# Optimization experiments

Measured on AMD Instinct MI355X. Metric: run time of the kernel, lower is better.

Reference implementation:

```python
import jax, jax.numpy as jnp
import numpy as np

T = 8          # number of adapter tasks
H = 1024       # hidden_size
I = 4096       # intermediate_size (bert dense input)
D = H // 16    # adapter bottleneck (reduction_factor=16)
B, S = 8, 512
EPS = 1e-12    # BERT LayerNorm eps


def _layernorm(x, g, b):
    mu = jnp.mean(x, axis=-1, keepdims=True)
    var = jnp.mean(jnp.square(x - mu), axis=-1, keepdims=True)
    return (x - mu) * jax.lax.rsqrt(var + EPS) * g + b


def setup_inputs() -> dict:
    key = jax.random.key(0)
    ks = jax.random.split(key, 14)
    std = 0.02
    inp = {
        "hidden_states": jax.random.normal(ks[0], (B, S, I), jnp.float32),
        "input_tensor": jax.random.normal(ks[1], (B, S, H), jnp.float32),
        "dense_w": jax.random.normal(ks[2], (H, I), jnp.float32) * std,
        "dense_b": jnp.zeros((H,), jnp.float32),
        "ln_g": jnp.ones((H,), jnp.float32),
        "ln_b": jnp.zeros((H,), jnp.float32),
        "down_w": jax.random.normal(ks[3], (T, D, H), jnp.float32) * std,
        "down_b": jnp.zeros((T, D), jnp.float32),
        "up_w": jax.random.normal(ks[4], (T, H, D), jnp.float32) * std,
        "up_b": jnp.zeros((T, H), jnp.float32),
        "key_w": jax.random.normal(ks[5], (H, H), jnp.float32) * std,
        "key_b": jnp.zeros((H,), jnp.float32),
        "query_w": jax.random.normal(ks[6], (H, H), jnp.float32) * std,
        "query_b": jnp.zeros((H,), jnp.float32),
        # value init: near-zero with identity diagonal
        "value_w": jnp.full((H, H), 1e-6, jnp.float32).at[jnp.arange(H), jnp.arange(H)].set(1.0),
    }
    return inp


def reference(hidden_states, input_tensor, dense_w, dense_b, ln_g, ln_b,
              down_w, down_b, up_w, up_b, key_w, key_b, query_w, query_b, value_w):
    # dense: [B,S,I] @ [H,I]^T -> [B,S,H]   (dropout = identity in eval)
    h = jnp.einsum('bsi,hi->bsh', hidden_states, dense_w) + dense_b
    prenorm = input_tensor + h
    adapter_in = _layernorm(prenorm, ln_g, ln_b)
    # batched per-task adapters: down-project, relu, up-project -> [T,B,S,H]
    down = jax.nn.relu(jnp.einsum('bsh,tdh->tbsd', adapter_in, down_w)
                       + down_b[:, None, None, :])
    adapter_out = jnp.einsum('tbsd,thd->tbsh', down, up_w) + up_b[:, None, None, :]
    # fusion attention over task axis T
    key = jnp.einsum('tbsh,kh->tbsk', adapter_out, key_w) + key_b
    value = jnp.einsum('tbsh,vh->tbsv', adapter_out + h[None], value_w)
    query = jnp.einsum('bsh,qh->bsq', prenorm, query_w) + query_b
    scores = jnp.sum(query[None] * key, axis=-1, keepdims=True)  # [T,B,S,1]
    probs = jax.nn.softmax(scores, axis=0)
    fusion = jnp.sum(probs * value, axis=0)                       # [B,S,H]
    return _layernorm(input_tensor + fusion, ln_g, ln_b)
```

## Files before the change

### kernel.cpp

```cpp
#include <hip/hip_runtime.h>
#include <cstdint>
#include <cstddef>

typedef float   f32x4 __attribute__((ext_vector_type(4)));
typedef _Float16 f16x8 __attribute__((ext_vector_type(8)));
typedef _Float16 f16x4 __attribute__((ext_vector_type(4)));

#define TOK  4096
#define HID  1024
#define IDIM 4096

#define GLDS16(gp, lp) __builtin_amdgcn_global_load_lds(                      \
    (const __attribute__((address_space(1))) void*)(gp),                      \
    (__attribute__((address_space(3))) void*)(lp), 16, 0, 0)


__global__ __launch_bounds__(256, 4) void gemm_dense(
    const _Float16* __restrict__ A, const _Float16* __restrict__ B,
    int K, int Kchunk, float* __restrict__ part, size_t zstride)
{
    __shared__ _Float16 lA[2][4096];
    __shared__ _Float16 lB[2][4096];
    const int tid  = threadIdx.x;
    const int lane = tid & 63;
    const int wave = tid >> 6;
    const int m0   = blockIdx.x * 128;
    const int n0   = blockIdx.y * 128;
    const int kz0  = blockIdx.z * Kchunk;
    const int wM   = (wave & 1) * 64;
    const int wN   = (wave >> 1) * 64;

    const int srow = lane >> 2;
    const int scol = ((lane & 3) ^ ((lane >> 3) & 3)) * 8;
    const _Float16* gA0 = A + (size_t)(m0 + wave * 32 + srow) * K + kz0 + scol;
    const _Float16* gA1 = gA0 + (size_t)16 * K;
    const _Float16* gB0 = B + (size_t)(n0 + wave * 32 + srow) * K + kz0 + scol;
    const _Float16* gB1 = gB0 + (size_t)16 * K;
    const int soff = wave * 1024;

    f32x4 acc[4][4] = {};
    const int fr  = lane & 15;
    const int khr = lane >> 4;
    const int kxo = (khr ^ ((fr >> 1) & 3)) * 8;

    GLDS16(gA0, &lA[0][soff]);
    GLDS16(gA1, &lA[0][soff + 512]);
    GLDS16(gB0, &lB[0][soff]);
    GLDS16(gB1, &lB[0][soff + 512]);
    __syncthreads();

    int cur = 0;
    for (int k = 0; k < Kchunk; k += 32) {
        if (k + 32 < Kchunk) {
            const int nb = cur ^ 1;
            GLDS16(gA0 + k + 32, &lA[nb][soff]);
            GLDS16(gA1 + k + 32, &lA[nb][soff + 512]);
            GLDS16(gB0 + k + 32, &lB[nb][soff]);
            GLDS16(gB1 + k + 32, &lB[nb][soff + 512]);
        }
        f16x8 afr[4], bfr[4];
#pragma unroll
        for (int mi = 0; mi < 4; ++mi)
            afr[mi] = *(const f16x8*)(&lA[cur][(wM + mi * 16 + fr) * 32 + kxo]);
#pragma unroll
        for (int ni = 0; ni < 4; ++ni)
            bfr[ni] = *(const f16x8*)(&lB[cur][(wN + ni * 16 + fr) * 32 + kxo]);
#pragma unroll
        for (int mi = 0; mi < 4; ++mi)
#pragma unroll
            for (int ni = 0; ni < 4; ++ni)
                acc[mi][ni] = __builtin_amdgcn_mfma_f32_16x16x32_f16(
                    afr[mi], bfr[ni], acc[mi][ni], 0, 0, 0);
        __syncthreads();
        cur ^= 1;
    }

    float* dst = part + (size_t)blockIdx.z * zstride;
    const int cn = lane & 15;
    const int rq = (lane >> 4) * 4;
#pragma unroll
    for (int mi = 0; mi < 4; ++mi)
#pragma unroll
        for (int r = 0; r < 4; ++r) {
            const int m = m0 + wM + mi * 16 + rq + r;
#pragma unroll
            for (int ni = 0; ni < 4; ++ni) {
                const int n = n0 + wN + ni * 16 + cn;
                dst[(size_t)m * HID + n] = acc[mi][ni][r];
            }
        }
}

__global__ __launch_bounds__(256) void reduce_sk(
    const float* __restrict__ in, size_t zstride4, int sk,
    _Float16* __restrict__ outp, int n4)
{
    const int gid = blockIdx.x * 256 + threadIdx.x;
    const int gsz = gridDim.x * 256;
    for (int i = gid; i < n4; i += gsz) {
        f32x4 v = ((const f32x4*)in)[i];
        for (int z = 1; z < sk; ++z)
            v += ((const f32x4*)in)[z * zstride4 + i];
        f16x4 o;
        o[0] = (_Float16)v[0]; o[1] = (_Float16)v[1];
        o[2] = (_Float16)v[2]; o[3] = (_Float16)v[3];
        ((f16x4*)outp)[i] = o;
    }
}

template <int MODE>
__global__ __launch_bounds__(1024, 4) void gemm_w32(
    const _Float16* __restrict__ Ah, const _Float16* __restrict__ B,
    int K, int Ncols,
    float* __restrict__ outF, _Float16* __restrict__ outH,
    const float* __restrict__ bias, const float* __restrict__ addv,
    const float* __restrict__ probs, const float* __restrict__ upb,
    const _Float16* __restrict__ A2, const _Float16* __restrict__ B2,
    _Float16* __restrict__ outH2)
{
    __shared__ _Float16 lA[2][8192];
    __shared__ _Float16 lB[2][8192];
    const int tid  = threadIdx.x;
    const int lane = tid & 63;
    const int wave = tid >> 6;
    const int m0   = blockIdx.x * 128;
    int n0, half = 0;
    const _Float16* Ap = Ah;
    const _Float16* Bp = B;
    if constexpr (MODE == 5) {
        half = blockIdx.y >> 2;
        n0 = (blockIdx.y & 3) * 128;
        if (half) { Ap = A2; Bp = B2; }
    } else {
        n0 = blockIdx.y * 128;
    }
    const int wM = (wave & 3) * 32;
    const int wN = (wave >> 2) * 32;

    f32x4 acc[2][2] = {};

    const int i8   = wave & 7;
    const int srow = lane >> 3;
    const int scol = ((lane & 7) ^ ((lane >> 3) & 7)) * 8;
    const _Float16* gsrc = ((wave < 8)
        ? Ap + (size_t)(m0 + i8 * 16 + srow) * K
        : Bp + (size_t)(n0 + i8 * 16 + srow) * K) + scol;
    const size_t g8K = (size_t)8 * K;
    _Float16* ldst = ((wave < 8) ? &lA[0][0] : &lB[0][0]) + i8 * 1024;

    const int fr  = lane & 15;
    const int khr = lane >> 4;

    GLDS16(gsrc, ldst);
    GLDS16(gsrc + g8K, ldst + 512);
    __syncthreads();

    int cur = 0;
    for (int k0 = 0; k0 < K; k0 += 64) {
        if (k0 + 64 < K) {
            _Float16* nd = ldst + (cur ^ 1) * 8192;
            GLDS16(gsrc + k0 + 64, nd);
            GLDS16(gsrc + k0 + 64 + g8K, nd + 512);
        }
#pragma unroll
        for (int kk = 0; kk < 2; ++kk) {
            f16x8 afr[2], bfr[2];
#pragma unroll
            for (int mi = 0; mi < 2; ++mi) {
                const int row = wM + mi * 16 + fr;
                afr[mi] = *(const f16x8*)(
                    &lA[cur][(row * 8 + ((kk * 4 + khr) ^ (row & 7))) * 8]);
            }
#pragma unroll
            for (int ni = 0; ni < 2; ++ni) {
                const int row = wN + ni * 16 + fr;
                bfr[ni] = *(const f16x8*)(
                    &lB[cur][(row * 8 + ((kk * 4 + khr) ^ (row & 7))) * 8]);
            }
#pragma unroll
            for (int mi = 0; mi < 2; ++mi)
#pragma unroll
                for (int ni = 0; ni < 2; ++ni)
                    acc[mi][ni] = __builtin_amdgcn_mfma_f32_16x16x32_f16(
                        afr[mi], bfr[ni], acc[mi][ni], 0, 0, 0);
        }
        __syncthreads();
        cur ^= 1;
    }

    const int cn = lane & 15;
    const int rq = (lane >> 4) * 4;
#pragma unroll
    for (int mi = 0; mi < 2; ++mi)
#pragma unroll
        for (int r = 0; r < 4; ++r) {
            const int m = m0 + wM + mi * 16 + rq + r;
#pragma unroll
            for (int ni = 0; ni < 2; ++ni) {
                const int n = n0 + wN + ni * 16 + cn;
                const float v = acc[mi][ni][r];
                if constexpr (MODE == 3) {
                    const size_t idx = (size_t)m * Ncols + n;
                    float s = v + addv[idx];
#pragma unroll
                    for (int t = 0; t < 8; ++t)
                        s += probs[(size_t)m * 8 + t] * upb[t * 1024 + n];
                    outH[idx] = (_Float16)s;
                } else if constexpr (MODE == 4) {
                    const size_t idx = (size_t)m * Ncols + n;
                    outF[idx] = v + addv[idx];
                } else {
                    const size_t idx = (size_t)m * 512 + n;
                    if (half == 0) {
                        const float y = v + bias[n];
                        outH[idx] = (_Float16)(y > 0.f ? y : 0.f);
                    } else {
                        outH2[idx] = (_Float16)(v + upb[n]);
                    }
                }
            }
        }
}

__global__ __launch_bounds__(256) void ln_fused(
    const float* __restrict__ part, int sk,
    const float* __restrict__ dbias, const float* __restrict__ it,
    const float* __restrict__ gam, const float* __restrict__ bet,
    float* __restrict__ h_f32, _Float16* __restrict__ ai, _Float16* __restrict__ pn)
{
    const int n = blockIdx.x, tid = threadIdx.x;
    const int lane = tid & 63, wave = tid >> 6;
    const size_t base = (size_t)n * 1024 + tid * 4;
    f32x4 h = *(const f32x4*)(dbias + tid * 4);
    for (int z = 0; z < sk; ++z)
        h += *(const f32x4*)(part + (size_t)z * TOK * HID + base);
    *(f32x4*)(h_f32 + base) = h;
    f32x4 x = h + *(const f32x4*)(it + base);
    float s = x[0] + x[1] + x[2] + x[3];
    float q = x[0] * x[0] + x[1] * x[1] + x[2] * x[2] + x[3] * x[3];
#pragma unroll
    for (int off = 1; off < 64; off <<= 1) {
        s += __shfl_xor(s, off);
        q += __shfl_xor(q, off);
    }
    __shared__ float rs[4], rq[4];
    if (lane == 0) { rs[wave] = s; rq[wave] = q; }
    __syncthreads();
    s = rs[0] + rs[1] + rs[2] + rs[3];
    q = rq[0] + rq[1] + rq[2] + rq[3];
    const float mu = s * (1.f / 1024.f);
    const float var = q * (1.f / 1024.f) - mu * mu;
    const float rstd = rsqrtf(var + 1e-12f);
    f32x4 gv = *(const f32x4*)(gam + tid * 4);
    f32x4 bv = *(const f32x4*)(bet + tid * 4);
    f16x4 av, pv;
#pragma unroll
    for (int j = 0; j < 4; ++j) {
        const float y = (x[j] - mu) * rstd * gv[j] + bv[j];
        av[j] = (_Float16)y;
        pv[j] = (_Float16)x[j];
    }
    *(f16x4*)(ai + base) = av;
    *(f16x4*)(pn + base) = pv;
}

__global__ __launch_bounds__(256) void ln_out(
    const float* __restrict__ fuse, const float* __restrict__ gam,
    const float* __restrict__ bet, float* __restrict__ outp)
{
    const int n = blockIdx.x, tid = threadIdx.x;
    const int lane = tid & 63, wave = tid >> 6;
    const size_t base = (size_t)n * 1024 + tid * 4;
    f32x4 x = *(const f32x4*)(fuse + base);
    float s = x[0] + x[1] + x[2] + x[3];
    float q = x[0] * x[0] + x[1] * x[1] + x[2] * x[2] + x[3] * x[3];
#pragma unroll
    for (int off = 1; off < 64; off <<= 1) {
        s += __shfl_xor(s, off);
        q += __shfl_xor(q, off);
    }
    __shared__ float rs[4], rq[4];
    if (lane == 0) { rs[wave] = s; rq[wave] = q; }
    __syncthreads();
    s = rs[0] + rs[1] + rs[2] + rs[3];
    q = rq[0] + rq[1] + rq[2] + rq[3];
    const float mu = s * (1.f / 1024.f);
    const float var = q * (1.f / 1024.f) - mu * mu;
    const float rstd = rsqrtf(var + 1e-12f);
    f32x4 gv = *(const f32x4*)(gam + tid * 4);
    f32x4 bv = *(const f32x4*)(bet + tid * 4);
    f32x4 y;
#pragma unroll
    for (int j = 0; j < 4; ++j) y[j] = (x[j] - mu) * rstd * gv[j] + bv[j];
    *(f32x4*)(outp + base) = y;
}

__global__ __launch_bounds__(256) void scores_softmax(
    const _Float16* __restrict__ pn, const float* __restrict__ WU,
    const float* __restrict__ cu,
    const _Float16* __restrict__ down, const _Float16* __restrict__ g,
    float* __restrict__ probs_out, _Float16* __restrict__ wdown)
{
    const int n = blockIdx.x, tid = threadIdx.x;
    const int lane = tid & 63, wave = tid >> 6;
    const _Float16* pnrow = pn + (size_t)n * 1024;
    float ub[8] = {};
#pragma unroll
    for (int j = 0; j < 4; ++j) {
        const int h = tid + j * 256;
        const float pv = (float)pnrow[h];
#pragma unroll
        for (int t = 0; t < 8; ++t) ub[t] += pv * WU[t * 1024 + h];
    }
#pragma unroll
    for (int off = 1; off < 64; off <<= 1) {
#pragma unroll
        for (int t = 0; t < 8; ++t) ub[t] += __shfl_xor(ub[t], off);
    }
    __shared__ float red[4][9];
    __shared__ float sd[8];
    __shared__ float pl[8];
    if (lane == 0) {
#pragma unroll
        for (int t = 0; t < 8; ++t) red[wave][t] = ub[t];
    }
    const int c0 = tid * 2;
    const size_t dbase = (size_t)n * 512;
    const float d0 = (float)down[dbase + c0];
    const float d1 = (float)down[dbase + c0 + 1];
    float pz = d0 * (float)g[dbase + c0] + d1 * (float)g[dbase + c0 + 1];
#pragma unroll
    for (int off = 1; off < 32; off <<= 1) pz += __shfl_xor(pz, off);
    if ((lane & 31) == 0) sd[wave * 2 + (lane >> 5)] = pz;
    __syncthreads();
    if (tid == 0) {
        float sc[8];
        float mx = -1e30f;
#pragma unroll
        for (int t = 0; t < 8; ++t) {
            sc[t] = sd[t] + cu[t] + red[0][t] + red[1][t] + red[2][t] + red[3][t];
            mx = fmaxf(mx, sc[t]);
        }
        float sum = 0.f;
#pragma unroll
        for (int t = 0; t < 8; ++t) { sc[t] = expf(sc[t] - mx); sum += sc[t]; }
        const float inv = 1.f / sum;
#pragma unroll
        for (int t = 0; t < 8; ++t) pl[t] = sc[t] * inv;
    }
    __syncthreads();
    const float pr = pl[c0 >> 6];
    wdown[dbase + c0]     = (_Float16)(pr * d0);
    wdown[dbase + c0 + 1] = (_Float16)(pr * d1);
    if (tid < 8) probs_out[(size_t)n * 8 + tid] = pl[tid];
}

__device__ inline void cvt_seg(const float* __restrict__ s, _Float16* __restrict__ d,
                               int n4, int gid, int gsz)
{
    for (int i = gid; i < n4; i += gsz) {
        f32x4 v = ((const f32x4*)s)[i];
        f16x4 o;
        o[0] = (_Float16)v[0]; o[1] = (_Float16)v[1];
        o[2] = (_Float16)v[2]; o[3] = (_Float16)v[3];
        ((f16x4*)d)[i] = o;
    }
}

__global__ __launch_bounds__(256) void convert4(
    const float* s0, _Float16* d0, int n0,
    const float* s1, _Float16* d1, int n1,
    const float* s2, _Float16* d2, int n2,
    const float* s3, _Float16* d3, int n3,
    float* bz)
{
    if (blockIdx.x == 0) {
        f32x4 z = {0.f, 0.f, 0.f, 0.f};
        *(f32x4*)(bz + threadIdx.x * 4) = z;
    }
    const int gid = blockIdx.x * 256 + threadIdx.x;
    const int gsz = gridDim.x * 256;
    cvt_seg(s0, d0, n0, gid, gsz);
    cvt_seg(s1, d1, n1, gid, gsz);
    cvt_seg(s2, d2, n2, gid, gsz);
    cvt_seg(s3, d3, n3, gid, gsz);
}

__global__ __launch_bounds__(256) void transpose_kw(
    const float* __restrict__ in, _Float16* __restrict__ outp,
    const float* __restrict__ rvec, float* __restrict__ rout)
{
    __shared__ float t[32][33];
    __shared__ float rpart[8][33];
    const int bx = blockIdx.x * 32;
    const int by = blockIdx.y * 32;
    const int tx = threadIdx.x & 31, ty = threadIdx.x >> 5;
#pragma unroll
    for (int j = 0; j < 32; j += 8)
        t[ty + j][tx] = in[(size_t)(by + ty + j) * 1024 + bx + tx];
    __syncthreads();
#pragma unroll
    for (int j = 0; j < 32; j += 8)
        outp[(size_t)(bx + ty + j) * 1024 + by + tx] = (_Float16)t[tx][ty + j];
    if (rvec) {
        float s = 0.f;
#pragma unroll
        for (int j = 0; j < 4; ++j) {
            const int k = ty * 4 + j;
            s += rvec[by + k] * t[k][tx];
        }
        rpart[ty][tx] = s;
        __syncthreads();
        if (ty == 0) {
            float v = rpart[0][tx];
#pragma unroll
            for (int r = 1; r < 8; ++r) v += rpart[r][tx];
            atomicAdd(rout + bx + tx, v);
        }
    }
}

__global__ __launch_bounds__(256) void reshape_up(
    const float* __restrict__ up_w, _Float16* __restrict__ upg,
    _Float16* __restrict__ upmix)
{
    const int i = blockIdx.x * 256 + threadIdx.x;
    const int d = i & 63;
    const int h = (i >> 6) & 1023;
    const int t = i >> 16;
    const float v = up_w[i];
    upg[(size_t)(t * 64 + d) * 1024 + h] = (_Float16)v;
    upmix[(size_t)h * 512 + t * 64 + d]  = (_Float16)v;
}

__global__ __launch_bounds__(256) void score_weights(
    const _Float16* __restrict__ wfuse, const _Float16* __restrict__ upg,
    const float* __restrict__ up_b, const float* __restrict__ bfuse,
    float* __restrict__ WU, float* __restrict__ bg, float* __restrict__ cu)
{
    const int b = blockIdx.x, tid = threadIdx.x;
    const int lane = tid & 63, wave = tid >> 6;
    __shared__ float red[4][8];
    if (b < 1024) {
        const f16x4 w = *(const f16x4*)(wfuse + (size_t)b * 1024 + tid * 4);
        float a[8] = {};
#pragma unroll
        for (int j = 0; j < 4; ++j) {
            const float wv = (float)w[j];
            const int hp = tid * 4 + j;
#pragma unroll
            for (int t = 0; t < 8; ++t) a[t] += wv * up_b[t * 1024 + hp];
        }
#pragma unroll
        for (int off = 1; off < 64; off <<= 1) {
#pragma unroll
            for (int t = 0; t < 8; ++t) a[t] += __shfl_xor(a[t], off);
        }
        if (lane == 0) {
#pragma unroll
            for (int t = 0; t < 8; ++t) red[wave][t] = a[t];
        }
        __syncthreads();
        if (tid < 8)
            WU[tid * 1024 + b] = red[0][tid] + red[1][tid] + red[2][tid] + red[3][tid];
    } else {
        float s;
        if (b < 1536) {
            const int td = b - 1024;
            const f16x4 w = *(const f16x4*)(upg + (size_t)td * 1024 + tid * 4);
            const f32x4 v = *(const f32x4*)(bfuse + tid * 4);
            s = (float)w[0] * v[0] + (float)w[1] * v[1]
              + (float)w[2] * v[2] + (float)w[3] * v[3];
        } else {
            const int t = b - 1536;
            const f32x4 u = *(const f32x4*)(up_b + (size_t)t * 1024 + tid * 4);
            const f32x4 v = *(const f32x4*)(bfuse + tid * 4);
            s = u[0] * v[0] + u[1] * v[1] + u[2] * v[2] + u[3] * v[3];
        }
#pragma unroll
        for (int off = 1; off < 64; off <<= 1) s += __shfl_xor(s, off);
        if (lane == 0) red[wave][0] = s;
        __syncthreads();
        if (tid == 0) {
            const float tot = red[0][0] + red[1][0] + red[2][0] + red[3][0];
            if (b < 1536) bg[b - 1024] = tot;
            else          cu[b - 1536] = tot;
        }
    }
}

extern "C" void kernel_launch(void* const* d_in, const int* in_sizes, int n_in,
                              void* d_out, int out_size, void* d_ws, size_t ws_size,
                              hipStream_t stream)
{
    const float* hs      = (const float*)d_in[0];
    const float* it      = (const float*)d_in[1];
    const float* dense_w = (const float*)d_in[2];
    const float* dense_b = (const float*)d_in[3];
    const float* ln_g    = (const float*)d_in[4];
    const float* ln_b    = (const float*)d_in[5];
    const float* down_w  = (const float*)d_in[6];
    const float* down_b  = (const float*)d_in[7];
    const float* up_w    = (const float*)d_in[8];
    const float* up_b    = (const float*)d_in[9];
    const float* key_w   = (const float*)d_in[10];
    const float* key_b   = (const float*)d_in[11];
    const float* query_w = (const float*)d_in[12];
    const float* query_b = (const float*)d_in[13];
    const float* value_w = (const float*)d_in[14];
    float* outp = (float*)d_out;
    (void)in_sizes; (void)n_in; (void)out_size; (void)key_b;

    const size_t MiB = 1ull << 20;
    char* p = (char*)d_ws;
    _Float16* w_dense  = (_Float16*)p; p += 8 * MiB;
    _Float16* w_queryT = (_Float16*)p; p += 2 * MiB;
    _Float16* w_keyT   = (_Float16*)p; p += 2 * MiB;
    _Float16* w_value  = (_Float16*)p; p += 2 * MiB;
    _Float16* w_fuseM  = (_Float16*)p; p += 2 * MiB;
    _Float16* w_wg     = (_Float16*)p; p += 1 * MiB;
    _Float16* w_down   = (_Float16*)p; p += 1 * MiB;
    _Float16* w_upg    = (_Float16*)p; p += 1 * MiB;
    _Float16* w_upmix  = (_Float16*)p; p += 1 * MiB;
    float*    bfuse    = (float*)p;    p += 1 * MiB;
    float*    WU       = bfuse + 1024;
    float*    bg       = WU + 8 * 1024;
    float*    cu       = bg + 512;
    float*    h_f32    = (float*)p;    p += 16 * MiB;
    _Float16* ai       = (_Float16*)p; p += 8 * MiB;
    _Float16* pn       = (_Float16*)p; p += 8 * MiB;
    _Float16* hs_h = (_Float16*)h_f32;
    char* rb = p;
    const int sk = (ws_size >= (size_t)(53 + 64) * MiB) ? 4 : 2;
    float*    prep  = (float*)rb;
    float*    part  = (float*)rb;
    _Float16* down  = (_Float16*)(rb + 16 * MiB);
    _Float16* g     = (_Float16*)(rb + 20 * MiB);
    _Float16* wdown = (_Float16*)(rb + 24 * MiB);
    float*    probs = (float*)(rb + 28 * MiB);
    float*    fuse  = (float*)rb;
    _Float16* mixed = ai;

    convert4<<<2048, 256, 0, stream>>>(hs, hs_h, TOK * IDIM / 4,
                                       dense_w, w_dense, HID * IDIM / 4,
                                       value_w, w_value, HID * HID / 4,
                                       down_w,  w_down,  512 * HID / 4,
                                       bfuse);
    transpose_kw<<<dim3(32, 32), 256, 0, stream>>>(key_w, w_keyT, query_b, bfuse);
    transpose_kw<<<dim3(32, 32), 256, 0, stream>>>(query_w, w_queryT, nullptr, nullptr);
    reshape_up<<<2048, 256, 0, stream>>>(up_w, w_upg, w_upmix);
    gemm_dense<<<dim3(8, 8, 4), 256, 0, stream>>>(
        w_queryT, w_keyT, HID, HID / 4, prep, (size_t)HID * HID);
    reduce_sk<<<1024, 256, 0, stream>>>(prep, (size_t)HID * HID / 4, 4,
                                        w_fuseM, HID * HID / 4);
    gemm_dense<<<dim3(4, 8, 4), 256, 0, stream>>>(
        w_upg, w_fuseM, HID, HID / 4, prep, (size_t)512 * HID);
    reduce_sk<<<512, 256, 0, stream>>>(prep, (size_t)512 * HID / 4, 4,
                                       w_wg, 512 * HID / 4);
    score_weights<<<1544, 256, 0, stream>>>(w_fuseM, w_upg, up_b, bfuse,
                                            WU, bg, cu);

    gemm_dense<<<dim3(32, 8, sk), 256, 0, stream>>>(
        hs_h, w_dense, IDIM, IDIM / sk, part, (size_t)TOK * HID);
    ln_fused<<<TOK, 256, 0, stream>>>(part, sk, dense_b, it, ln_g, ln_b, h_f32, ai, pn);
    gemm_w32<5><<<dim3(32, 8), 1024, 0, stream>>>(
        ai, w_down, HID, 512, nullptr, down, down_b, nullptr, nullptr, bg,
        pn, w_wg, g);
    scores_softmax<<<TOK, 256, 0, stream>>>(pn, WU, cu, down, g, probs, wdown);
    gemm_w32<3><<<dim3(32, 8), 1024, 0, stream>>>(
        wdown, w_upmix, 512, HID, nullptr, mixed, nullptr, h_f32, probs, up_b,
        nullptr, nullptr, nullptr);
    gemm_w32<4><<<dim3(32, 8), 1024, 0, stream>>>(
        mixed, w_value, HID, HID, fuse, nullptr, nullptr, it, nullptr, nullptr,
        nullptr, nullptr, nullptr);
    ln_out<<<TOK, 256, 0, stream>>>(fuse, ln_g, ln_b, outp);
}
```

Baseline: 338.9 us.

## Fold up-projection into value weight and fuse last two GEMMs

```diff
diff --git a/kernel.cpp b/kernel.cpp
--- a/kernel.cpp
+++ b/kernel.cpp
@@ -17,7 +17,7 @@
 
 __global__ __launch_bounds__(256, 4) void gemm_dense(
     const _Float16* __restrict__ A, const _Float16* __restrict__ B,
-    int K, int Kchunk, float* __restrict__ part, size_t zstride)
+    int K, int Kchunk, float* __restrict__ part, size_t zstride, int nstride)
 {
     __shared__ _Float16 lA[2][4096];
     __shared__ _Float16 lB[2][4096];
@@ -86,7 +86,7 @@
 #pragma unroll
             for (int ni = 0; ni < 4; ++ni) {
                 const int n = n0 + wN + ni * 16 + cn;
-                dst[(size_t)m * HID + n] = acc[mi][ni][r];
+                dst[(size_t)m * nstride + n] = acc[mi][ni][r];
             }
         }
 }
@@ -105,6 +105,34 @@
         o[0] = (_Float16)v[0]; o[1] = (_Float16)v[1];
         o[2] = (_Float16)v[2]; o[3] = (_Float16)v[3];
         ((f16x4*)outp)[i] = o;
+    }
+}
+
+__device__ __forceinline__ void mma64(
+    const _Float16* __restrict__ lAc, const _Float16* __restrict__ lBc,
+    int wM, int wN, int fr, int khr, f32x4 acc[2][2])
+{
+#pragma unroll
+    for (int kk = 0; kk < 2; ++kk) {
+        f16x8 afr[2], bfr[2];
+#pragma unroll
+        for (int mi = 0; mi < 2; ++mi) {
+            const int row = wM + mi * 16 + fr;
+            afr[mi] = *(const f16x8*)(
+                &lAc[(row * 8 + ((kk * 4 + khr) ^ (row & 7))) * 8]);
+        }
+#pragma unroll
+        for (int ni = 0; ni < 2; ++ni) {
+            const int row = wN + ni * 16 + fr;
+            bfr[ni] = *(const f16x8*)(
+                &lBc[(row * 8 + ((kk * 4 + khr) ^ (row & 7))) * 8]);
+        }
+#pragma unroll
+        for (int mi = 0; mi < 2; ++mi)
+#pragma unroll
+            for (int ni = 0; ni < 2; ++ni)
+                acc[mi][ni] = __builtin_amdgcn_mfma_f32_16x16x32_f16(
+                    afr[mi], bfr[ni], acc[mi][ni], 0, 0, 0);
     }
 }
 
@@ -142,50 +170,47 @@
     const int i8   = wave & 7;
     const int srow = lane >> 3;
     const int scol = ((lane & 7) ^ ((lane >> 3) & 7)) * 8;
-    const _Float16* gsrc = ((wave < 8)
-        ? Ap + (size_t)(m0 + i8 * 16 + srow) * K
-        : Bp + (size_t)(n0 + i8 * 16 + srow) * K) + scol;
-    const size_t g8K = (size_t)8 * K;
     _Float16* ldst = ((wave < 8) ? &lA[0][0] : &lB[0][0]) + i8 * 1024;
-
     const int fr  = lane & 15;
     const int khr = lane >> 4;
 
-    GLDS16(gsrc, ldst);
-    GLDS16(gsrc + g8K, ldst + 512);
-    __syncthreads();
-
     int cur = 0;
-    for (int k0 = 0; k0 < K; k0 += 64) {
-        if (k0 + 64 < K) {
-            _Float16* nd = ldst + (cur ^ 1) * 8192;
-            GLDS16(gsrc + k0 + 64, nd);
-            GLDS16(gsrc + k0 + 64 + g8K, nd + 512);
-        }
-#pragma unroll
-        for (int kk = 0; kk < 2; ++kk) {
-            f16x8 afr[2], bfr[2];
-#pragma unroll
-            for (int mi = 0; mi < 2; ++mi) {
-                const int row = wM + mi * 16 + fr;
-                afr[mi] = *(const f16x8*)(
-                    &lA[cur][(row * 8 + ((kk * 4 + khr) ^ (row & 7))) * 8]);
+    {
+        const _Float16* gsrc = ((wave < 8)
+            ? Ap + (size_t)(m0 + i8 * 16 + srow) * K
+            : Bp + (size_t)(n0 + i8 * 16 + srow) * K) + scol;
+        const size_t g8K = (size_t)8 * K;
+        GLDS16(gsrc, ldst);
+        GLDS16(gsrc + g8K, ldst + 512);
+        __syncthreads();
+        for (int k0 = 0; k0 < K; k0 += 64) {
+            if (k0 + 64 < K) {
+                _Float16* nd = ldst + (cur ^ 1) * 8192;
+                GLDS16(gsrc + k0 + 64, nd);
+                GLDS16(gsrc + k0 + 64 + g8K, nd + 512);
             }
-#pragma unroll
-            for (int ni = 0; ni < 2; ++ni) {
-                const int row = wN + ni * 16 + fr;
-                bfr[ni] = *(const f16x8*)(
-                    &lB[cur][(row * 8 + ((kk * 4 + khr) ^ (row & 7))) * 8]);
+            mma64(&lA[cur][0], &lB[cur][0], wM, wN, fr, khr, acc);
+            __syncthreads();
+            cur ^= 1;
+        }
+    }
+    if constexpr (MODE == 6) {
+        const _Float16* gsrc = ((wave < 8)
+            ? A2 + (size_t)(m0 + i8 * 16 + srow) * 512
+            : B2 + (size_t)(n0 + i8 * 16 + srow) * 512) + scol;
+        GLDS16(gsrc, ldst + cur * 8192);
+        GLDS16(gsrc + 8 * 512, ldst + cur * 8192 + 512);
+        __syncthreads();
+        for (int k0 = 0; k0 < 512; k0 += 64) {
+            if (k0 + 64 < 512) {
+                _Float16* nd = ldst + (cur ^ 1) * 8192;
+                GLDS16(gsrc + k0 + 64, nd);
+                GLDS16(gsrc + k0 + 64 + 8 * 512, nd + 512);
             }
-#pragma unroll
-            for (int mi = 0; mi < 2; ++mi)
-#pragma unroll
-                for (int ni = 0; ni < 2; ++ni)
-                    acc[mi][ni] = __builtin_amdgcn_mfma_f32_16x16x32_f16(
-                        afr[mi], bfr[ni], acc[mi][ni], 0, 0, 0);
-        }
-        __syncthreads();
-        cur ^= 1;
+            mma64(&lA[cur][0], &lB[cur][0], wM, wN, fr, khr, acc);
+            __syncthreads();
+            cur ^= 1;
+        }
     }
 
     const int cn = lane & 15;
@@ -195,20 +220,22 @@
 #pragma unroll
         for (int r = 0; r < 4; ++r) {
             const int m = m0 + wM + mi * 16 + rq + r;
+            float pr8[8];
+            if constexpr (MODE == 6) {
+#pragma unroll
+                for (int t = 0; t < 8; ++t) pr8[t] = probs[(size_t)m * 8 + t];
+            }
 #pragma unroll
             for (int ni = 0; ni < 2; ++ni) {
                 const int n = n0 + wN + ni * 16 + cn;
                 const float v = acc[mi][ni][r];
-                if constexpr (MODE == 3) {
+                if constexpr (MODE == 6) {
                     const size_t idx = (size_t)m * Ncols + n;
                     float s = v + addv[idx];
 #pragma unroll
                     for (int t = 0; t < 8; ++t)
-                        s += probs[(size_t)m * 8 + t] * upb[t * 1024 + n];
-                    outH[idx] = (_Float16)s;
-                } else if constexpr (MODE == 4) {
-                    const size_t idx = (size_t)m * Ncols + n;
-                    outF[idx] = v + addv[idx];
+                        s += pr8[t] * upb[t * 1024 + n];
+                    outF[idx] = s;
                 } else {
                     const size_t idx = (size_t)m * 512 + n;
                     if (half == 0) {
@@ -226,7 +253,7 @@
     const float* __restrict__ part, int sk,
     const float* __restrict__ dbias, const float* __restrict__ it,
     const float* __restrict__ gam, const float* __restrict__ bet,
-    float* __restrict__ h_f32, _Float16* __restrict__ ai, _Float16* __restrict__ pn)
+    _Float16* __restrict__ hh, _Float16* __restrict__ ai, _Float16* __restrict__ pn)
 {
     const int n = blockIdx.x, tid = threadIdx.x;
     const int lane = tid & 63, wave = tid >> 6;
@@ -234,7 +261,10 @@
     f32x4 h = *(const f32x4*)(dbias + tid * 4);
     for (int z = 0; z < sk; ++z)
         h += *(const f32x4*)(part + (size_t)z * TOK * HID + base);
-    *(f32x4*)(h_f32 + base) = h;
+    f16x4 hv;
+#pragma unroll
+    for (int j = 0; j < 4; ++j) hv[j] = (_Float16)h[j];
+    *(f16x4*)(hh + base) = hv;
     f32x4 x = h + *(const f32x4*)(it + base);
     float s = x[0] + x[1] + x[2] + x[3];
     float q = x[0] * x[0] + x[1] * x[1] + x[2] * x[2] + x[3] * x[3];
@@ -386,63 +416,69 @@
     cvt_seg(s3, d3, n3, gid, gsz);
 }
 
-__global__ __launch_bounds__(256) void transpose_kw(
-    const float* __restrict__ in, _Float16* __restrict__ outp,
-    const float* __restrict__ rvec, float* __restrict__ rout)
+__global__ __launch_bounds__(256) void prep_misc(
+    const float* __restrict__ key_w, _Float16* __restrict__ w_keyT,
+    const float* __restrict__ query_w, _Float16* __restrict__ w_queryT,
+    const float* __restrict__ query_b, float* __restrict__ bfuse,
+    const float* __restrict__ up_w, _Float16* __restrict__ upg)
 {
     __shared__ float t[32][33];
     __shared__ float rpart[8][33];
-    const int bx = blockIdx.x * 32;
-    const int by = blockIdx.y * 32;
-    const int tx = threadIdx.x & 31, ty = threadIdx.x >> 5;
-#pragma unroll
-    for (int j = 0; j < 32; j += 8)
-        t[ty + j][tx] = in[(size_t)(by + ty + j) * 1024 + bx + tx];
-    __syncthreads();
-#pragma unroll
-    for (int j = 0; j < 32; j += 8)
-        outp[(size_t)(bx + ty + j) * 1024 + by + tx] = (_Float16)t[tx][ty + j];
-    if (rvec) {
-        float s = 0.f;
-#pragma unroll
-        for (int j = 0; j < 4; ++j) {
-            const int k = ty * 4 + j;
-            s += rvec[by + k] * t[k][tx];
-        }
-        rpart[ty][tx] = s;
+    const int b = blockIdx.x;
+    if (b < 2048) {
+        const int bb = (b < 1024) ? b : b - 1024;
+        const int bx = (bb & 31) * 32;
+        const int by = (bb >> 5) * 32;
+        const float* in = (b < 1024) ? key_w : query_w;
+        _Float16* outp  = (b < 1024) ? w_keyT : w_queryT;
+        const int tx = threadIdx.x & 31, ty = threadIdx.x >> 5;
+#pragma unroll
+        for (int j = 0; j < 32; j += 8)
+            t[ty + j][tx] = in[(size_t)(by + ty + j) * 1024 + bx + tx];
         __syncthreads();
-        if (ty == 0) {
-            float v = rpart[0][tx];
-#pragma unroll
-            for (int r = 1; r < 8; ++r) v += rpart[r][tx];
-            atomicAdd(rout + bx + tx, v);
-        }
-    }
-}
-
-__global__ __launch_bounds__(256) void reshape_up(
-    const float* __restrict__ up_w, _Float16* __restrict__ upg,
-    _Float16* __restrict__ upmix)
-{
-    const int i = blockIdx.x * 256 + threadIdx.x;
-    const int d = i & 63;
-    const int h = (i >> 6) & 1023;
-    const int t = i >> 16;
-    const float v = up_w[i];
-    upg[(size_t)(t * 64 + d) * 1024 + h] = (_Float16)v;
-    upmix[(size_t)h * 512 + t * 64 + d]  = (_Float16)v;
+#pragma unroll
+        for (int j = 0; j < 32; j += 8)
+            outp[(size_t)(bx + ty + j) * 1024 + by + tx] = (_Float16)t[tx][ty + j];
+        if (b < 1024) {
+            float s = 0.f;
+#pragma unroll
+            for (int j = 0; j < 4; ++j) {
+                const int k = ty * 4 + j;
+                s += query_b[by + k] * t[k][tx];
+            }
+            rpart[ty][tx] = s;
+            __syncthreads();
+            if (ty == 0) {
+                float v = rpart[0][tx];
+#pragma unroll
+                for (int r = 1; r < 8; ++r) v += rpart[r][tx];
+                atomicAdd(bfuse + bx + tx, v);
+            }
+        }
+    } else {
+        const int i = (b - 2048) * 256 + threadIdx.x;
+        const int d = i & 63;
+        const int h = (i >> 6) & 1023;
+        const int t8 = i >> 16;
+        upg[(size_t)(t8 * 64 + d) * 1024 + h] = (_Float16)up_w[i];
+    }
 }
 
 __global__ __launch_bounds__(256) void score_weights(
-    const _Float16* __restrict__ wfuse, const _Float16* __restrict__ upg,
-    const float* __restrict__ up_b, const float* __restrict__ bfuse,
-    float* __restrict__ WU, float* __restrict__ bg, float* __restrict__ cu)
+    const _Float16* __restrict__ wfuse, const _Float16* __restrict__ wval,
+    const _Float16* __restrict__ upg, const float* __restrict__ up_b,
+    const float* __restrict__ bfuse,
+    float* __restrict__ WU, float* __restrict__ BVU,
+    float* __restrict__ bg, float* __restrict__ cu)
 {
     const int b = blockIdx.x, tid = threadIdx.x;
     const int lane = tid & 63, wave = tid >> 6;
     __shared__ float red[4][8];
-    if (b < 1024) {
-        const f16x4 w = *(const f16x4*)(wfuse + (size_t)b * 1024 + tid * 4);
+    if (b < 2048) {
+        const _Float16* row = (b < 1024)
+            ? wfuse + (size_t)b * 1024
+            : wval  + (size_t)(b - 1024) * 1024;
+        const f16x4 w = *(const f16x4*)(row + tid * 4);
         float a[8] = {};
 #pragma unroll
         for (int j = 0; j < 4; ++j) {
@@ -461,18 +497,21 @@
             for (int t = 0; t < 8; ++t) red[wave][t] = a[t];
         }
         __syncthreads();
-        if (tid < 8)
-            WU[tid * 1024 + b] = red[0][tid] + red[1][tid] + red[2][tid] + red[3][tid];
+        if (tid < 8) {
+            const float tot = red[0][tid] + red[1][tid] + red[2][tid] + red[3][tid];
+            if (b < 1024) WU[tid * 1024 + b] = tot;
+            else          BVU[tid * 1024 + (b - 1024)] = tot;
+        }
     } else {
         float s;
-        if (b < 1536) {
-            const int td = b - 1024;
+        if (b < 2560) {
+            const int td = b - 2048;
             const f16x4 w = *(const f16x4*)(upg + (size_t)td * 1024 + tid * 4);
             const f32x4 v = *(const f32x4*)(bfuse + tid * 4);
             s = (float)w[0] * v[0] + (float)w[1] * v[1]
               + (float)w[2] * v[2] + (float)w[3] * v[3];
         } else {
-            const int t = b - 1536;
+            const int t = b - 2560;
             const f32x4 u = *(const f32x4*)(up_b + (size_t)t * 1024 + tid * 4);
             const f32x4 v = *(const f32x4*)(bfuse + tid * 4);
             s = u[0] * v[0] + u[1] * v[1] + u[2] * v[2] + u[3] * v[3];
@@ -483,8 +522,8 @@
         __syncthreads();
         if (tid == 0) {
             const float tot = red[0][0] + red[1][0] + red[2][0] + red[3][0];
-            if (b < 1536) bg[b - 1024] = tot;
-            else          cu[b - 1536] = tot;
+            if (b < 2560) bg[b - 2048] = tot;
+            else          cu[b - 2560] = tot;
         }
     }
 }
@@ -519,17 +558,19 @@
     _Float16* w_value  = (_Float16*)p; p += 2 * MiB;
     _Float16* w_fuseM  = (_Float16*)p; p += 2 * MiB;
     _Float16* w_wg     = (_Float16*)p; p += 1 * MiB;
+    _Float16* w_wvu    = (_Float16*)p; p += 1 * MiB;
     _Float16* w_down   = (_Float16*)p; p += 1 * MiB;
     _Float16* w_upg    = (_Float16*)p; p += 1 * MiB;
-    _Float16* w_upmix  = (_Float16*)p; p += 1 * MiB;
     float*    bfuse    = (float*)p;    p += 1 * MiB;
     float*    WU       = bfuse + 1024;
     float*    bg       = WU + 8 * 1024;
     float*    cu       = bg + 512;
-    float*    h_f32    = (float*)p;    p += 16 * MiB;
+    float*    BVU      = cu + 8;
+    char*     hslot    = p;            p += 16 * MiB;
+    _Float16* h_h      = (_Float16*)hslot;
     _Float16* ai       = (_Float16*)p; p += 8 * MiB;
     _Float16* pn       = (_Float16*)p; p += 8 * MiB;
-    _Float16* hs_h = (_Float16*)h_f32;
+    _Float16* hs_h = (_Float16*)hslot;
     char* rb = p;
     const int sk = (ws_size >= (size_t)(53 + 64) * MiB) ? 4 : 2;
     float*    prep  = (float*)rb;
@@ -539,39 +580,39 @@
     _Float16* wdown = (_Float16*)(rb + 24 * MiB);
     float*    probs = (float*)(rb + 28 * MiB);
     float*    fuse  = (float*)rb;
-    _Float16* mixed = ai;
 
     convert4<<<2048, 256, 0, stream>>>(hs, hs_h, TOK * IDIM / 4,
                                        dense_w, w_dense, HID * IDIM / 4,
                                        value_w, w_value, HID * HID / 4,
                                        down_w,  w_down,  512 * HID / 4,
                                        bfuse);
-    transpose_kw<<<dim3(32, 32), 256, 0, stream>>>(key_w, w_keyT, query_b, bfuse);
-    transpose_kw<<<dim3(32, 32), 256, 0, stream>>>(query_w, w_queryT, nullptr, nullptr);
-    reshape_up<<<2048, 256, 0, stream>>>(up_w, w_upg, w_upmix);
+    prep_misc<<<4096, 256, 0, stream>>>(key_w, w_keyT, query_w, w_queryT,
+                                        query_b, bfuse, up_w, w_upg);
+    gemm_dense<<<dim3(8, 4, 4), 256, 0, stream>>>(
+        w_value, w_upg, HID, HID / 4, prep, (size_t)HID * 512, 512);
+    reduce_sk<<<512, 256, 0, stream>>>(prep, (size_t)HID * 512 / 4, 4,
+                                       w_wvu, HID * 512 / 4);
     gemm_dense<<<dim3(8, 8, 4), 256, 0, stream>>>(
-        w_queryT, w_keyT, HID, HID / 4, prep, (size_t)HID * HID);
+        w_queryT, w_keyT, HID, HID / 4, prep, (size_t)HID * HID, 1024);
     reduce_sk<<<1024, 256, 0, stream>>>(prep, (size_t)HID * HID / 4, 4,
                                         w_fuseM, HID * HID / 4);
     gemm_dense<<<dim3(4, 8, 4), 256, 0, stream>>>(
-        w_upg, w_fuseM, HID, HID / 4, prep, (size_t)512 * HID);
+        w_upg, w_fuseM, HID, HID / 4, prep, (size_t)512 * HID, 1024);
     reduce_sk<<<512, 256, 0, stream>>>(prep, (size_t)512 * HID / 4, 4,
                                        w_wg, 512 * HID / 4);
-    score_weights<<<1544, 256, 0, stream>>>(w_fuseM, w_upg, up_b, bfuse,
-                                            WU, bg, cu);
+    score_weights<<<2568, 256, 0, stream>>>(w_fuseM, w_value, w_upg, up_b,
+                                            bfuse, WU, BVU, bg, cu);
 
     gemm_dense<<<dim3(32, 8, sk), 256, 0, stream>>>(
-        hs_h, w_dense, IDIM, IDIM / sk, part, (size_t)TOK * HID);
-    ln_fused<<<TOK, 256, 0, stream>>>(part, sk, dense_b, it, ln_g, ln_b, h_f32, ai, pn);
+        hs_h, w_dense, IDIM, IDIM / sk, part, (size_t)TOK * HID, 1024);
+    ln_fused<<<TOK, 256, 0, stream>>>(part, sk, dense_b, it, ln_g, ln_b,
+                                      h_h, ai, pn);
     gemm_w32<5><<<dim3(32, 8), 1024, 0, stream>>>(
         ai, w_down, HID, 512, nullptr, down, down_b, nullptr, nullptr, bg,
         pn, w_wg, g);
     scores_softmax<<<TOK, 256, 0, stream>>>(pn, WU, cu, down, g, probs, wdown);
-    gemm_w32<3><<<dim3(32, 8), 1024, 0, stream>>>(
-        wdown, w_upmix, 512, HID, nullptr, mixed, nullptr, h_f32, probs, up_b,
-        nullptr, nullptr, nullptr);
-    gemm_w32<4><<<dim3(32, 8), 1024, 0, stream>>>(
-        mixed, w_value, HID, HID, fuse, nullptr, nullptr, it, nullptr, nullptr,
-        nullptr, nullptr, nullptr);
+    gemm_w32<6><<<dim3(32, 8), 1024, 0, stream>>>(
+        h_h, w_value, HID, HID, fuse, nullptr, nullptr, it, probs, BVU,
+        wdown, w_wvu, nullptr);
     ln_out<<<TOK, 256, 0, stream>>>(fuse, ln_g, ln_b, outp);
 }
```

New measurement: 343.1 us. No clear change (+1.3%).
